# Kernel tuning notes

Hardware: AMD Instinct MI355X
Metric: run time of the kernel (lower is better)

## Reference

```python
import jax, jax.numpy as jnp
import numpy as np

N = 8192
HID = 64
TAU = 0.8
LAMBDA = 0.5
POS_DENSITY = 0.005


def setup_inputs() -> dict:
    key = jax.random.key(0)
    k1, k2, k3, k4, k5, k6, k7 = jax.random.split(key, 7)
    x1 = jax.random.normal(k1, (N, HID), dtype=jnp.float32)
    x2 = jax.random.normal(k2, (N, HID), dtype=jnp.float32)
    # xavier_uniform with gain=1.414 for square [HID, HID] linears
    limit = 1.414 * np.sqrt(6.0 / (HID + HID))
    W1 = jax.random.uniform(k3, (HID, HID), dtype=jnp.float32, minval=-limit, maxval=limit)
    b1 = jnp.zeros((HID,), dtype=jnp.float32)
    W2 = jax.random.uniform(k4, (HID, HID), dtype=jnp.float32, minval=-limit, maxval=limit)
    b2 = jnp.zeros((HID,), dtype=jnp.float32)
    pm = (jax.random.uniform(k5, (N, N), dtype=jnp.float32) < POS_DENSITY).astype(jnp.float32)
    positive_matrix = jnp.maximum(pm, jnp.eye(N, dtype=jnp.float32))
    return {"x1": x1, "x2": x2, "W1": W1, "b1": b1, "W2": W2, "b2": b2,
            "positive_matrix": positive_matrix}


def _project(x, W1, b1, W2, b2):
    # nn.Linear(hidden, hidden) -> ELU -> nn.Linear(hidden, hidden)
    h = jax.nn.elu(x @ W1.T + b1)
    return h @ W2.T + b2


def _l2norm(z, eps=1e-12):
    # F.normalize(p=2, dim=1): x / max(||x||, eps)
    n = jnp.linalg.norm(z, axis=-1, keepdims=True)
    return z / jnp.maximum(n, eps)


def _sim(z1, z2, tau):
    return jnp.exp((_l2norm(z1) @ _l2norm(z2).T) / tau)  # [N, N]


def _masked_loss(sim_mat, pos):
    row = sim_mat / (jnp.sum(sim_mat, axis=-1, keepdims=True) + 1e-8)
    return -jnp.log(jnp.sum(row * pos, axis=-1) + 1e-8).mean()


def reference(x1, x2, W1, b1, W2, b2, positive_matrix):
    z1 = _project(x1, W1, b1, W2, b2)
    z2 = _project(x2, W1, b1, W2, b2)
    sc_mp = _sim(z1, z2, TAU)
    mp_sc = _sim(z2, z1, TAU)
    sc_loss = _masked_loss(sc_mp, positive_matrix)
    mp_loss = _masked_loss(mp_sc, positive_matrix)
    return sc_loss * LAMBDA + mp_loss * (1.0 - LAMBDA)
```

## Files before the change

kernel.cpp:

```cpp
#include <hip/hip_runtime.h>
#include <hip/hip_bf16.h>

#define N 8192
#define HID 64
#define JC 8

typedef __attribute__((ext_vector_type(4))) float f32x4;
typedef __attribute__((ext_vector_type(8))) __bf16 bf16x8;

__device__ __forceinline__ void gload_lds16(const void* g, float* l) {
  __builtin_amdgcn_global_load_lds(
      (const __attribute__((address_space(1))) void*)g,
      (__attribute__((address_space(3))) void*)l, 16, 0, 0);
}

__global__ __launch_bounds__(256) void proj_kernel(
    const float* __restrict__ x1, const float* __restrict__ x2,
    const float* __restrict__ W1, const float* __restrict__ b1,
    const float* __restrict__ W2, const float* __restrict__ b2,
    __bf16* __restrict__ Z1h, __bf16* __restrict__ Z2h,
    float* __restrict__ stats)
{
  __shared__ __align__(16) float w1s[64*68];
  __shared__ __align__(16) float w2s[64*68];
  __shared__ __align__(16) float xs[4][64];
  __shared__ __align__(16) float hs[4][64];

  const int tid  = threadIdx.x;
  const int lane = tid & 63;
  const int w    = tid >> 6;

  int gtid = blockIdx.x * 256 + tid;
  if (gtid < 4*N) stats[gtid] = 0.f;

  for (int idx = tid; idx < 64*64; idx += 256) {
    int j = idx >> 6, k = idx & 63;
    w1s[j*68+k] = W1[idx];
    w2s[j*68+k] = W2[idx];
  }
  __syncthreads();

  const float bias1 = b1[lane];
  const float bias2 = b2[lane];

  const int wave_global = blockIdx.x * 4 + w;
  #pragma unroll 1
  for (int it = 0; it < 4; ++it) {
    int R = wave_global * 4 + it;
    const float* src; __bf16* dst;
    if (R < N) { src = x1 + (size_t)R*HID;      dst = Z1h + (size_t)R*HID; }
    else       { src = x2 + (size_t)(R-N)*HID;  dst = Z2h + (size_t)(R-N)*HID; }

    float xv = src[lane];
    xs[w][lane] = xv;
    float acc = bias1;
    #pragma unroll
    for (int qq = 0; qq < 16; ++qq) {
      f32x4 xq = *(const f32x4*)&xs[w][qq*4];
      f32x4 wq = *(const f32x4*)&w1s[lane*68 + qq*4];
      acc += xq.x*wq.x + xq.y*wq.y + xq.z*wq.z + xq.w*wq.w;
    }
    float h = acc > 0.f ? acc : expm1f(acc);
    hs[w][lane] = h;
    float acc2 = bias2;
    #pragma unroll
    for (int qq = 0; qq < 16; ++qq) {
      f32x4 hq = *(const f32x4*)&hs[w][qq*4];
      f32x4 wq = *(const f32x4*)&w2s[lane*68 + qq*4];
      acc2 += hq.x*wq.x + hq.y*wq.y + hq.z*wq.z + hq.w*wq.w;
    }
    float z = acc2;
    float ss = z*z;
    #pragma unroll
    for (int m = 1; m < 64; m <<= 1) ss += __shfl_xor(ss, m);
    float inv = 1.0f / fmaxf(sqrtf(ss), 1e-12f);
    dst[lane] = (__bf16)(z * inv);
  }
}

__global__ __launch_bounds__(256, 4) void sim_kernel(
    const __bf16* __restrict__ Z1h, const __bf16* __restrict__ Z2h,
    const float* __restrict__ pos,
    float* __restrict__ rowsum1, float* __restrict__ num1,
    float* __restrict__ rowsum2, float* __restrict__ num2)
{
  __shared__ __align__(16) float zs1[2][2048];
  __shared__ __align__(16) float zs2[2][2048];

  const int tid  = threadIdx.x;
  const int lane = tid & 63;
  const int w    = tid >> 6;
  const int r16  = lane & 15;
  const int q    = lane >> 4;

  const int bi  = blockIdx.x / JC;
  const int jc  = blockIdx.x % JC;
  const int i0  = bi*64 + w*16;

  const __bf16* z1r = Z1h + (size_t)(i0 + r16)*HID + q*8;
  const __bf16* z2r = Z2h + (size_t)(i0 + r16)*HID + q*8;
  const bf16x8 a1lo = *(const bf16x8*)(z1r);
  const bf16x8 a1hi = *(const bf16x8*)(z1r + 32);
  const bf16x8 a2lo = *(const bf16x8*)(z2r);
  const bf16x8 a2hi = *(const bf16x8*)(z2r + 32);

  float s1 = 0.f, n1 = 0.f, s2 = 0.f, n2 = 0.f;

  const int jbeg = jc * (N/JC);
  const float Cexp = 1.8033688011112042f;
  const float* prow = pos + (size_t)(i0 + r16)*N + q*4;

  f32x4 PA0, PA1, PA2, PA3, PB0, PB1, PB2, PB3, PC0, PC1, PC2, PC3;

#define STAGEZ(BUF, JJ) { \
    const int r8 = lane >> 3; \
    const int sl = (lane & 7) ^ r8; \
    gload_lds16(Z1h + (size_t)((JJ) + w*16     + r8)*HID + sl*8, &zs1[BUF][(w*16    )*32]); \
    gload_lds16(Z1h + (size_t)((JJ) + w*16 + 8 + r8)*HID + sl*8, &zs1[BUF][(w*16 + 8)*32]); \
    gload_lds16(Z2h + (size_t)((JJ) + w*16     + r8)*HID + sl*8, &zs2[BUF][(w*16    )*32]); \
    gload_lds16(Z2h + (size_t)((JJ) + w*16 + 8 + r8)*HID + sl*8, &zs2[BUF][(w*16 + 8)*32]); \
  }

#define LOADPOS(P, JJ) { \
    P##0 = *(const f32x4*)(prow + (JJ)); \
    P##1 = *(const f32x4*)(prow + (JJ) + 16); \
    P##2 = *(const f32x4*)(prow + (JJ) + 32); \
    P##3 = *(const f32x4*)(prow + (JJ) + 48); \
  }

#define COMPC(BUF, C, CC, PV) { \
    const int R  = (CC) + (C)*16 + r16; \
    const int sw = r16 & 7; \
    bf16x8 b2lo = *(const bf16x8*)&zs2[BUF][R*32 + ((q    ) ^ sw)*4]; \
    bf16x8 b2hi = *(const bf16x8*)&zs2[BUF][R*32 + ((q + 4) ^ sw)*4]; \
    bf16x8 b1lo = *(const bf16x8*)&zs1[BUF][R*32 + ((q    ) ^ sw)*4]; \
    bf16x8 b1hi = *(const bf16x8*)&zs1[BUF][R*32 + ((q + 4) ^ sw)*4]; \
    f32x4 zero4 = {0.f,0.f,0.f,0.f}; \
    f32x4 d1 = __builtin_amdgcn_mfma_f32_16x16x32_bf16(b2lo, a1lo, zero4, 0,0,0); \
    d1       = __builtin_amdgcn_mfma_f32_16x16x32_bf16(b2hi, a1hi, d1,    0,0,0); \
    f32x4 d2 = __builtin_amdgcn_mfma_f32_16x16x32_bf16(b1lo, a2lo, zero4, 0,0,0); \
    d2       = __builtin_amdgcn_mfma_f32_16x16x32_bf16(b1hi, a2hi, d2,    0,0,0); \
    _Pragma("unroll") \
    for (int r = 0; r < 4; ++r) { \
      float e1 = exp2f(d1[r] * Cexp); \
      float e2 = exp2f(d2[r] * Cexp); \
      s1 += e1; n1 += e1 * PV[r]; \
      s2 += e2; n2 += e2 * PV[r]; \
    } }

#define STEP(BUF, P) { COMPC(BUF,0,0,P##0) COMPC(BUF,1,0,P##1) COMPC(BUF,0,32,P##2) COMPC(BUF,1,32,P##3) }

#define PHASE(TB, TBN, PLOAD, PCONS, TT) { \
    STAGEZ(TBN, jbeg + ((TT)+1)*64) \
    LOADPOS(PLOAD, jbeg + ((TT)+2)*64) \
    STEP(TB, PCONS) \
    asm volatile("s_waitcnt vmcnt(4)" ::: "memory"); \
    __builtin_amdgcn_s_barrier(); \
  }

  STAGEZ(0, jbeg)
  LOADPOS(PA, jbeg)
  LOADPOS(PB, jbeg + 64)
  asm volatile("s_waitcnt vmcnt(4)" ::: "memory");
  __builtin_amdgcn_s_barrier();

  #pragma unroll 1
  for (int g = 0; g < 2; ++g) {
    const int t0 = g*6;
    PHASE(0, 1, PC, PA, t0+0)
    PHASE(1, 0, PA, PB, t0+1)
    PHASE(0, 1, PB, PC, t0+2)
    PHASE(1, 0, PC, PA, t0+3)
    PHASE(0, 1, PA, PB, t0+4)
    PHASE(1, 0, PB, PC, t0+5)
  }
  PHASE(0, 1, PC, PA, 12)
  PHASE(1, 0, PA, PB, 13)
  STAGEZ(1, jbeg + 15*64)
  STEP(0, PC)
  asm volatile("s_waitcnt vmcnt(0)" ::: "memory");
  __builtin_amdgcn_s_barrier();
  STEP(1, PA)

#undef STAGEZ
#undef LOADPOS
#undef COMPC
#undef STEP
#undef PHASE

  s1 += __shfl_xor(s1, 16); s1 += __shfl_xor(s1, 32);
  n1 += __shfl_xor(n1, 16); n1 += __shfl_xor(n1, 32);
  s2 += __shfl_xor(s2, 16); s2 += __shfl_xor(s2, 32);
  n2 += __shfl_xor(n2, 16); n2 += __shfl_xor(n2, 32);

  if (lane < 16) {
    int row = i0 + r16;
    atomicAdd(&rowsum1[row], s1);
    atomicAdd(&num1[row],    n1);
    atomicAdd(&rowsum2[row], s2);
    atomicAdd(&num2[row],    n2);
  }
}

__global__ __launch_bounds__(1024) void loss_kernel(
    const float* __restrict__ rowsum1, const float* __restrict__ num1,
    const float* __restrict__ rowsum2, const float* __restrict__ num2,
    float* __restrict__ out)
{
  __shared__ float part[16];
  const int tid = threadIdx.x, lane = tid & 63, w = tid >> 6;
  float acc = 0.f;
  for (int i = tid; i < N; i += 1024) {
    float sc = -logf(num1[i]/(rowsum1[i]+1e-8f) + 1e-8f);
    float mp = -logf(num2[i]/(rowsum2[i]+1e-8f) + 1e-8f);
    acc += 0.5f*sc + 0.5f*mp;
  }
  #pragma unroll
  for (int m = 1; m < 64; m <<= 1) acc += __shfl_xor(acc, m);
  if (lane == 0) part[w] = acc;
  __syncthreads();
  if (tid == 0) {
    float t = 0.f;
    #pragma unroll
    for (int k = 0; k < 16; ++k) t += part[k];
    out[0] = t * (1.0f/N);
  }
}

extern "C" void kernel_launch(void* const* d_in, const int* in_sizes, int n_in,
                              void* d_out, int out_size, void* d_ws, size_t ws_size,
                              hipStream_t stream) {
  const float* x1  = (const float*)d_in[0];
  const float* x2  = (const float*)d_in[1];
  const float* W1  = (const float*)d_in[2];
  const float* b1  = (const float*)d_in[3];
  const float* W2  = (const float*)d_in[4];
  const float* b2  = (const float*)d_in[5];
  const float* pos = (const float*)d_in[6];

  char* ws = (char*)d_ws;
  __bf16* Z1h = (__bf16*)ws;
  __bf16* Z2h = (__bf16*)(ws + (size_t)N*HID*sizeof(__bf16));
  size_t zbytes = (size_t)2*N*HID*sizeof(__bf16);
  float* rowsum1 = (float*)(ws + zbytes);
  float* num1    = rowsum1 + N;
  float* rowsum2 = num1 + N;
  float* num2    = rowsum2 + N;

  proj_kernel<<<1024, 256, 0, stream>>>(x1, x2, W1, b1, W2, b2, Z1h, Z2h, rowsum1);
  sim_kernel<<<128*JC, 256, 0, stream>>>(Z1h, Z2h, pos, rowsum1, num1, rowsum2, num2);
  loss_kernel<<<1, 1024, 0, stream>>>(rowsum1, num1, rowsum2, num2, (float*)d_out);
}
```

Measured before the change: 422.9 us.

## Pack positive matrix into bitmask in a pre-pass and consume bits in sim kernel

Adds a pre-pass kernel that reads the dense float positive matrix and packs each group of four entries into a 4-bit byte. The similarity kernel then loads one 32-bit word per lane per 64-column tile and shares it via lane shuffles, instead of four float4 loads. Masked accumulation becomes a predicated add rather than a multiply. This lightens register pressure and memory traffic inside the compute-heavy kernel. The full dense matrix is still read every call, and there is an extra kernel launch plus a mask write and read.

```diff
diff --git a/kernel.cpp b/kernel.cpp
--- a/kernel.cpp
+++ b/kernel.cpp
@@ -12,6 +12,21 @@
   __builtin_amdgcn_global_load_lds(
       (const __attribute__((address_space(1))) void*)g,
       (__attribute__((address_space(3))) void*)l, 16, 0, 0);
+}
+
+__global__ __launch_bounds__(256) void mask_kernel(
+    const float* __restrict__ pos, unsigned char* __restrict__ mask)
+{
+  int idx = blockIdx.x * 256 + threadIdx.x;
+  const int stride = 2048 * 256;
+  #pragma unroll 1
+  for (int it = 0; it < 32; ++it) {
+    int i = idx + it * stride;
+    f32x4 v = *(const f32x4*)(pos + (size_t)i * 4);
+    unsigned b = (unsigned)(v.x != 0.f) | ((unsigned)(v.y != 0.f) << 1)
+               | ((unsigned)(v.z != 0.f) << 2) | ((unsigned)(v.w != 0.f) << 3);
+    mask[i] = (unsigned char)b;
+  }
 }
 
 __global__ __launch_bounds__(256) void proj_kernel(
@@ -80,7 +95,7 @@
 
 __global__ __launch_bounds__(256, 4) void sim_kernel(
     const __bf16* __restrict__ Z1h, const __bf16* __restrict__ Z2h,
-    const float* __restrict__ pos,
+    const unsigned char* __restrict__ mask,
     float* __restrict__ rowsum1, float* __restrict__ num1,
     float* __restrict__ rowsum2, float* __restrict__ num2)
 {
@@ -108,9 +123,9 @@
 
   const int jbeg = jc * (N/JC);
   const float Cexp = 1.8033688011112042f;
-  const float* prow = pos + (size_t)(i0 + r16)*N + q*4;
-
-  f32x4 PA0, PA1, PA2, PA3, PB0, PB1, PB2, PB3, PC0, PC1, PC2, PC3;
+  const unsigned char* mrowq = mask + (size_t)(i0 + r16) * (N/4) + q*4;
+
+  unsigned MA, MB, MC;
 
 #define STAGEZ(BUF, JJ) { \
     const int r8 = lane >> 3; \
@@ -121,14 +136,9 @@
     gload_lds16(Z2h + (size_t)((JJ) + w*16 + 8 + r8)*HID + sl*8, &zs2[BUF][(w*16 + 8)*32]); \
   }
 
-#define LOADPOS(P, JJ) { \
-    P##0 = *(const f32x4*)(prow + (JJ)); \
-    P##1 = *(const f32x4*)(prow + (JJ) + 16); \
-    P##2 = *(const f32x4*)(prow + (JJ) + 32); \
-    P##3 = *(const f32x4*)(prow + (JJ) + 48); \
-  }
-
-#define COMPC(BUF, C, CC, PV) { \
+#define LOADM(P, JJ) { P = *(const unsigned*)(mrowq + ((JJ) >> 2)); }
+
+#define COMPC(BUF, C, CC, MK) { \
     const int R  = (CC) + (C)*16 + r16; \
     const int sw = r16 & 7; \
     bf16x8 b2lo = *(const bf16x8*)&zs2[BUF][R*32 + ((q    ) ^ sw)*4]; \
@@ -144,46 +154,51 @@
     for (int r = 0; r < 4; ++r) { \
       float e1 = exp2f(d1[r] * Cexp); \
       float e2 = exp2f(d2[r] * Cexp); \
-      s1 += e1; n1 += e1 * PV[r]; \
-      s2 += e2; n2 += e2 * PV[r]; \
+      s1 += e1; s2 += e2; \
+      if ((MK >> (8*q + r)) & 1u) { n1 += e1; n2 += e2; } \
     } }
 
-#define STEP(BUF, P) { COMPC(BUF,0,0,P##0) COMPC(BUF,1,0,P##1) COMPC(BUF,0,32,P##2) COMPC(BUF,1,32,P##3) }
-
-#define PHASE(TB, TBN, PLOAD, PCONS, TT) { \
+#define STEP(BUF, MB_) { \
+    const unsigned Mk0 = __shfl((int)MB_,      r16); \
+    const unsigned Mk1 = __shfl((int)MB_, 16 + r16); \
+    const unsigned Mk2 = __shfl((int)MB_, 32 + r16); \
+    const unsigned Mk3 = __shfl((int)MB_, 48 + r16); \
+    COMPC(BUF,0,0,Mk0) COMPC(BUF,1,0,Mk1) COMPC(BUF,0,32,Mk2) COMPC(BUF,1,32,Mk3) }
+
+#define PHASE(TB, TBN, MLOAD, MCONS, TT) { \
     STAGEZ(TBN, jbeg + ((TT)+1)*64) \
-    LOADPOS(PLOAD, jbeg + ((TT)+2)*64) \
-    STEP(TB, PCONS) \
-    asm volatile("s_waitcnt vmcnt(4)" ::: "memory"); \
+    LOADM(MLOAD, jbeg + ((TT)+2)*64) \
+    STEP(TB, MCONS) \
+    asm volatile("s_waitcnt vmcnt(1)" ::: "memory"); \
     __builtin_amdgcn_s_barrier(); \
   }
 
   STAGEZ(0, jbeg)
-  LOADPOS(PA, jbeg)
-  LOADPOS(PB, jbeg + 64)
-  asm volatile("s_waitcnt vmcnt(4)" ::: "memory");
+  LOADM(MA, jbeg)
+  LOADM(MB, jbeg + 64)
+  asm volatile("s_waitcnt vmcnt(1)" ::: "memory");
   __builtin_amdgcn_s_barrier();
 
   #pragma unroll 1
   for (int g = 0; g < 2; ++g) {
     const int t0 = g*6;
-    PHASE(0, 1, PC, PA, t0+0)
-    PHASE(1, 0, PA, PB, t0+1)
-    PHASE(0, 1, PB, PC, t0+2)
-    PHASE(1, 0, PC, PA, t0+3)
-    PHASE(0, 1, PA, PB, t0+4)
-    PHASE(1, 0, PB, PC, t0+5)
-  }
-  PHASE(0, 1, PC, PA, 12)
-  PHASE(1, 0, PA, PB, 13)
+    PHASE(0, 1, MC, MA, t0+0)
+    PHASE(1, 0, MA, MB, t0+1)
+    PHASE(0, 1, MB, MC, t0+2)
+    PHASE(1, 0, MC, MA, t0+3)
+    PHASE(0, 1, MA, MB, t0+4)
+    PHASE(1, 0, MB, MC, t0+5)
+  }
+  PHASE(0, 1, MC, MA, 12)
+  PHASE(1, 0, MA, MB, 13)
   STAGEZ(1, jbeg + 15*64)
-  STEP(0, PC)
+  STEP(0, MC)
   asm volatile("s_waitcnt vmcnt(0)" ::: "memory");
   __builtin_amdgcn_s_barrier();
-  STEP(1, PA)
+  STEP(1, MA)
 
 #undef STAGEZ
-#undef LOADPOS
+#undef LOADM
 #undef COMPC
 #undef STEP
 #undef PHASE
@@ -246,8 +261,10 @@
   float* num1    = rowsum1 + N;
   float* rowsum2 = num1 + N;
   float* num2    = rowsum2 + N;
-
+  unsigned char* mask = (unsigned char*)(ws + zbytes + (size_t)4*N*sizeof(float));
+
+  mask_kernel<<<2048, 256, 0, stream>>>(pos, mask);
   proj_kernel<<<1024, 256, 0, stream>>>(x1, x2, W1, b1, W2, b2, Z1h, Z2h, rowsum1);
-  sim_kernel<<<128*JC, 256, 0, stream>>>(Z1h, Z2h, pos, rowsum1, num1, rowsum2, num2);
+  sim_kernel<<<128*JC, 256, 0, stream>>>(Z1h, Z2h, mask, rowsum1, num1, rowsum2, num2);
   loss_kernel<<<1, 1024, 0, stream>>>(rowsum1, num1, rowsum2, num2, (float*)d_out);
 }
```

Result: slower. 439.1 us (+3.8%).
